# Kernel tuning notes

Measured on AMD Instinct MI355X. Metric: run time of the kernel, lower is better.

## Reference

```python
import jax, jax.numpy as jnp
import numpy as np

HID = 2048
NH = 16
NKV = 4
HD = 256
ROT = 64  # partial_rotary_factor 0.25 * 256
EPS = 1e-6
B, S = 2, 2048


def rms_norm(x, w, eps=EPS):
    # Qwen3.5 RMSNorm: zero-init weight, (1 + w) scaling, fp32 compute
    xf = x.astype(jnp.float32)
    out = xf * jax.lax.rsqrt(jnp.mean(xf * xf, axis=-1, keepdims=True) + eps)
    return (out * (1.0 + w.astype(jnp.float32))).astype(x.dtype)


def rotate_half(x):
    x1, x2 = jnp.split(x, 2, axis=-1)
    return jnp.concatenate([-x2, x1], axis=-1)


def apply_partial_rope(q, k, cos, sin):
    # q,k: [b,h,s,d]; cos,sin: [b,s,rot] -> unsqueeze head dim
    c = cos[:, None, :, :]
    s = sin[:, None, :, :]
    q_rot, q_pass = q[..., :ROT], q[..., ROT:]
    k_rot, k_pass = k[..., :ROT], k[..., ROT:]
    q_rot = q_rot * c + rotate_half(q_rot) * s
    k_rot = k_rot * c + rotate_half(k_rot) * s
    return (jnp.concatenate([q_rot, q_pass], -1), jnp.concatenate([k_rot, k_pass], -1))


def setup_inputs() -> dict:
    key = jax.random.key(0)
    ks = jax.random.split(key, 10)
    hidden_states = jax.random.normal(ks[0], (B, S, HID), jnp.float32)
    # rotary embeddings over ROT dims (half freqs duplicated, HF-style)
    inv_freq = 1.0 / (10000.0 ** (np.arange(0, ROT, 2, dtype=np.float32) / ROT))
    t = np.arange(S, dtype=np.float32)
    freqs = np.outer(t, inv_freq)  # [S, ROT/2]
    emb = np.concatenate([freqs, freqs], axis=-1)  # [S, ROT]
    cos = jnp.broadcast_to(jnp.cos(emb)[None], (B, S, ROT)).astype(jnp.float32)
    sin = jnp.broadcast_to(jnp.sin(emb)[None], (B, S, ROT)).astype(jnp.float32)
    # additive causal mask
    m = jnp.where(jnp.tril(jnp.ones((S, S), bool)), 0.0, -1e9).astype(jnp.float32)
    attention_mask = jnp.broadcast_to(m[None, None], (B, 1, S, S))
    sc = 0.02
    Wq = jax.random.normal(ks[1], (HID, NH * HD * 2), jnp.float32) * sc
    Wk = jax.random.normal(ks[2], (HID, NKV * HD), jnp.float32) * sc
    Wv = jax.random.normal(ks[3], (HID, NKV * HD), jnp.float32) * sc
    Wo = jax.random.normal(ks[4], (NH * HD, HID), jnp.float32) * sc
    q_norm_w = jax.random.normal(ks[5], (HD,), jnp.float32) * sc
    k_norm_w = jax.random.normal(ks[6], (HD,), jnp.float32) * sc
    Wr = jax.random.normal(ks[7], (HID, 2 * HD), jnp.float32) * sc  # dynamic router
    return {"hidden_states": hidden_states, "cos": cos, "sin": sin,
            "attention_mask": attention_mask, "Wq": Wq, "Wk": Wk, "Wv": Wv,
            "Wo": Wo, "q_norm_w": q_norm_w, "k_norm_w": k_norm_w, "Wr": Wr}


def reference(hidden_states, cos, sin, attention_mask, Wq, Wk, Wv, Wo, q_norm_w, k_norm_w, Wr):
    b, s, _ = hidden_states.shape
    # dynamic router -> per-token virtual gates (inner_head for q/k, inner_head_v for v)
    vectors = jax.nn.sigmoid(hidden_states @ Wr)           # [b,s,2*HD]
    g_qk, g_v = jnp.split(vectors, 2, axis=-1)             # [b,s,HD] each
    # fused q projection -> query + sigmoid output gate
    qkv = (hidden_states @ Wq).reshape(b, s, NH, 2 * HD)
    q, gate = jnp.split(qkv, 2, axis=-1)                   # [b,s,NH,HD]
    gate = gate.reshape(b, s, NH * HD)
    k = (hidden_states @ Wk).reshape(b, s, NKV, HD)
    v = (hidden_states @ Wv).reshape(b, s, NKV, HD)
    # per-head RMSNorm before RoPE
    q = rms_norm(q, q_norm_w)
    k = rms_norm(k, k_norm_w)
    q = q.transpose(0, 2, 1, 3)                            # [b,NH,s,HD]
    k = k.transpose(0, 2, 1, 3)                            # [b,NKV,s,HD]
    v = v.transpose(0, 2, 1, 3)
    # virtual gating (inner_head): per-token per-channel gate within each head
    q = q * g_qk[:, None, :, :]
    k = k * g_qk[:, None, :, :]
    v = v * g_v[:, None, :, :]
    # partial RoPE on first ROT dims
    q, k = apply_partial_rope(q, k, cos, sin)
    # GQA: repeat kv heads
    n_rep = NH // NKV
    k = jnp.repeat(k, n_rep, axis=1)                       # [b,NH,s,HD]
    v = jnp.repeat(v, n_rep, axis=1)
    scores = jnp.einsum('bhqd,bhkd->bhqk', q, k) / jnp.sqrt(jnp.float32(HD))
    scores = scores + attention_mask
    attn = jax.nn.softmax(scores.astype(jnp.float32), axis=-1).astype(q.dtype)
    out = jnp.einsum('bhqk,bhkd->bhqd', attn, v)
    out = out.transpose(0, 2, 1, 3).reshape(b, s, NH * HD)
    out = out * jax.nn.sigmoid(gate)                       # sigmoid output gate
    return out @ Wo
```

## Files before the change

### kernel.cpp

```cpp
#include <hip/hip_runtime.h>

#define S_LEN 2048
#define NB    2
#define NH    16
#define NKV   4
#define HDIM  256
#define LW    10752

using bf16x8 = __attribute__((ext_vector_type(8))) short;
using s16x4  = __attribute__((ext_vector_type(4))) short;
using f32x4  = __attribute__((ext_vector_type(4))) float;

__device__ __forceinline__ float bf2f(short u){
  union { float f; unsigned u; } x; x.u = ((unsigned)(unsigned short)u) << 16; return x.f;
}
__device__ __forceinline__ short f2bf(float f){
  unsigned i = __builtin_bit_cast(unsigned, f);
  unsigned r = (i + 0x7fffu + ((i >> 16) & 1u)) >> 16;
  return (short)r;
}
__device__ __forceinline__ float sigm(float x){ return 1.0f / (1.0f + __expf(-x)); }

__device__ __forceinline__ void gload16(const short* g, short* lds){
  __builtin_amdgcn_global_load_lds((const __attribute__((address_space(1))) void*)g,
                                   (__attribute__((address_space(3))) void*)lds,
                                   16, 0, 0);
}

__global__ void k_cvt(const float* __restrict__ in, short* __restrict__ out, int n4){
  int i = blockIdx.x * blockDim.x + threadIdx.x;
  if (i >= n4) return;
  float4 v = ((const float4*)in)[i];
  s16x4 o;
  o[0] = f2bf(v.x); o[1] = f2bf(v.y); o[2] = f2bf(v.z); o[3] = f2bf(v.w);
  ((s16x4*)out)[i] = o;
}

__global__ void k_add(const float* __restrict__ b, float* __restrict__ o, int n4){
  int i = blockIdx.x * blockDim.x + threadIdx.x;
  const int stride = gridDim.x * blockDim.x;
  for (; i < n4; i += stride) {
    float4 x = ((const float4*)o)[i];
    float4 y = ((const float4*)b)[i];
    float4 z = {x.x + y.x, x.y + y.y, x.z + y.z, x.w + y.w};
    ((float4*)o)[i] = z;
  }
}

__global__ void k_wt(const float* __restrict__ Wq, const float* __restrict__ Wk,
                     const float* __restrict__ Wv, const float* __restrict__ Wr,
                     const float* __restrict__ Wo, short* __restrict__ WcatT,
                     short* __restrict__ WoT)
{
  __shared__ float tile[32][33];
  const int id = blockIdx.x;
  const float* src; short* dst; int R, C, Ct, local;
  if (id < 16384)      { src = Wq; dst = WcatT;                      R = 2048; C = 8192; Ct = 256; local = id; }
  else if (id < 18432) { src = Wk; dst = WcatT + (size_t)8192*2048;  R = 2048; C = 1024; Ct =  32; local = id - 16384; }
  else if (id < 20480) { src = Wv; dst = WcatT + (size_t)9216*2048;  R = 2048; C = 1024; Ct =  32; local = id - 18432; }
  else if (id < 21504) { src = Wr; dst = WcatT + (size_t)10240*2048; R = 2048; C =  512; Ct =  16; local = id - 20480; }
  else                 { src = Wo; dst = WoT;                        R = 4096; C = 2048; Ct =  64; local = id - 21504; }
  const int c0 = (local % Ct) * 32, r0 = (local / Ct) * 32;
  const int tx = threadIdx.x, ty = threadIdx.y;
  #pragma unroll
  for (int i = ty; i < 32; i += 8)
    tile[i][tx] = src[(size_t)(r0 + i) * C + c0 + tx];
  __syncthreads();
  #pragma unroll
  for (int i = ty; i < 32; i += 8)
    dst[(size_t)(c0 + i) * R + r0 + tx] = f2bf(tile[tx][i]);
}

__global__ void k_vt(const short* __restrict__ Ycat, short* __restrict__ VT){
  __shared__ short tile[32][33];
  int b = blockIdx.z >> 2, hk = blockIdx.z & 3;
  int s0 = blockIdx.x * 32, d0 = blockIdx.y * 32;
  int tx = threadIdx.x, ty = threadIdx.y;
  #pragma unroll
  for (int i = ty; i < 32; i += 8)
    tile[i][tx] = Ycat[(size_t)(b * S_LEN + s0 + i) * LW + 9216 + hk * 256 + d0 + tx];
  __syncthreads();
  #pragma unroll
  for (int i = ty; i < 32; i += 8)
    VT[(size_t)((b * NKV + hk) * HDIM + d0 + i) * S_LEN + s0 + tx] = tile[tx][i];
}

#define MFMA_(a, b, c) __builtin_amdgcn_mfma_f32_16x16x32_bf16(a, b, c, 0, 0, 0)
#define As ((short(*)[2][8192])(SMEM))
#define Bs ((short(*)[2][8192])(SMEM + 32768))
#define LDA_(buf, ks, mh, f) (*(const bf16x8*)&As[buf][ks][(wm*128 + (mh)*64 + (f)*16 + l15) * 32 + rdSlot])
#define LDB_(buf, ks, f)     (*(const bf16x8*)&Bs[buf][ks][(wn*64  + (f)*16 + l15) * 32 + rdSlot])
#define STAGE_A_(buf, ks, tile) { \
  gload16(aG0 + (size_t)(tile)*64 + (ks)*32, &As[buf][ks][w*512]); \
  gload16(aG1 + (size_t)(tile)*64 + (ks)*32, &As[buf][ks][4096 + w*512]); }
#define STAGE_B_(buf, ks, tile) { \
  gload16(bG0 + (size_t)(tile)*64 + (ks)*32, &Bs[buf][ks][w*512]); \
  gload16(bG1 + (size_t)(tile)*64 + (ks)*32, &Bs[buf][ks][4096 + w*512]); }
#define VM4 asm volatile("s_waitcnt vmcnt(4)" ::: "memory");
#define PH_(buf, ks, mh, LB, ...) { \
  bf16x8 a0 = LDA_(buf,ks,mh,0), a1 = LDA_(buf,ks,mh,1), a2 = LDA_(buf,ks,mh,2), a3 = LDA_(buf,ks,mh,3); \
  if (LB) { b0 = LDB_(buf,ks,0); b1 = LDB_(buf,ks,1); b2 = LDB_(buf,ks,2); b3 = LDB_(buf,ks,3); } \
  __VA_ARGS__ \
  __builtin_amdgcn_s_barrier(); \
  asm volatile("s_waitcnt lgkmcnt(0)" ::: "memory"); \
  __builtin_amdgcn_s_setprio(1); \
  acc[(mh)*4+0][0] = MFMA_(a0, b0, acc[(mh)*4+0][0]); \
  acc[(mh)*4+0][1] = MFMA_(a0, b1, acc[(mh)*4+0][1]); \
  acc[(mh)*4+0][2] = MFMA_(a0, b2, acc[(mh)*4+0][2]); \
  acc[(mh)*4+0][3] = MFMA_(a0, b3, acc[(mh)*4+0][3]); \
  acc[(mh)*4+1][0] = MFMA_(a1, b0, acc[(mh)*4+1][0]); \
  acc[(mh)*4+1][1] = MFMA_(a1, b1, acc[(mh)*4+1][1]); \
  acc[(mh)*4+1][2] = MFMA_(a1, b2, acc[(mh)*4+1][2]); \
  acc[(mh)*4+1][3] = MFMA_(a1, b3, acc[(mh)*4+1][3]); \
  acc[(mh)*4+2][0] = MFMA_(a2, b0, acc[(mh)*4+2][0]); \
  acc[(mh)*4+2][1] = MFMA_(a2, b1, acc[(mh)*4+2][1]); \
  acc[(mh)*4+2][2] = MFMA_(a2, b2, acc[(mh)*4+2][2]); \
  acc[(mh)*4+2][3] = MFMA_(a2, b3, acc[(mh)*4+2][3]); \
  acc[(mh)*4+3][0] = MFMA_(a3, b0, acc[(mh)*4+3][0]); \
  acc[(mh)*4+3][1] = MFMA_(a3, b1, acc[(mh)*4+3][1]); \
  acc[(mh)*4+3][2] = MFMA_(a3, b2, acc[(mh)*4+3][2]); \
  acc[(mh)*4+3][3] = MFMA_(a3, b3, acc[(mh)*4+3][3]); \
  __builtin_amdgcn_s_setprio(0); \
  __builtin_amdgcn_s_barrier(); }

template<int OUTF32, int CM, int SPLITK>
__global__ __launch_bounds__(512) void k_gemm2(const short* __restrict__ A,
                                               const short* __restrict__ BT,
                                               void* __restrict__ C0,
                                               void* __restrict__ C1,
                                               int M, int N, int Kpitch, int Klen,
                                               int gx)
{
  __shared__ __align__(16) short SMEM[65536];
  const int t = threadIdx.x, lane = t & 63, w = t >> 6;
  const int l15 = lane & 15;
  const int wm = w >> 2, wn = w & 3;
  const int rdSlot = (((lane >> 4) ^ ((lane >> 1) & 3)) * 8);

  const int nwg = gridDim.x;
  const int swz = (blockIdx.x & 7) * (nwg >> 3) + (blockIdx.x >> 3);
  int rem = swz, kOff = 0;
  void* Cp = C0;
  if (SPLITK) {
    rem = swz & 127;
    if (swz >> 7) { kOff = Klen; Cp = C1; }
  }
  const int m0 = (CM ? (rem % gx) : (rem / gx)) * 256;
  const int n0 = (CM ? (rem / gx) : (rem % gx)) * 256;

  const int sRow = w * 16 + (lane >> 2);
  const int sSwz = ((lane & 3) ^ ((lane >> 3) & 3)) * 8;
  const short* aG0 = A  + (size_t)(m0 + sRow) * Kpitch + kOff + sSwz;
  const short* aG1 = A  + (size_t)(m0 + 128 + sRow) * Kpitch + kOff + sSwz;
  const short* bG0 = BT + (size_t)(n0 + sRow) * Kpitch + kOff + sSwz;
  const short* bG1 = BT + (size_t)(n0 + 128 + sRow) * Kpitch + kOff + sSwz;

  f32x4 acc[8][4] = {};
  bf16x8 b0 = {}, b1 = {}, b2 = {}, b3 = {};

  STAGE_A_(0, 0, 0) STAGE_A_(0, 1, 0) STAGE_B_(0, 0, 0) STAGE_B_(0, 1, 0)
  STAGE_A_(1, 0, 1) STAGE_B_(1, 0, 1)
  asm volatile("s_waitcnt vmcnt(4)" ::: "memory");
  __builtin_amdgcn_s_barrier();

  const int nIt = Klen >> 7;
  for (int i = 0; i < nIt; ++i) {
    const int c = 2 * i;
    const bool st = (i + 1 < nIt);
    PH_(0, 0, 0, 1, STAGE_A_(1, 1, c + 1))
    PH_(0, 0, 1, 0, STAGE_B_(1, 1, c + 1))
    PH_(0, 1, 0, 1, if (st) STAGE_A_(0, 0, c + 2))
    PH_(0, 1, 1, 0, if (st) STAGE_B_(0, 0, c + 2) VM4)
    PH_(1, 0, 0, 1, if (st) STAGE_A_(0, 1, c + 2))
    PH_(1, 0, 1, 0, if (st) STAGE_B_(0, 1, c + 2))
    PH_(1, 1, 0, 1, if (st) STAGE_A_(1, 0, c + 3))
    PH_(1, 1, 1, 0, if (st) STAGE_B_(1, 0, c + 3) VM4)
  }

  float* Cl = (float*)SMEM;
  const int g = lane >> 4;
  #pragma unroll
  for (int ch = 0; ch < 4; ++ch) {
    if (wm == (ch >> 1)) {
      #pragma unroll
      for (int ii2 = 0; ii2 < 4; ++ii2)
        #pragma unroll
        for (int j = 0; j < 4; ++j)
          #pragma unroll
          for (int r = 0; r < 4; ++r)
            Cl[(ii2*16 + g*4 + r) * 260 + wn*64 + j*16 + l15] = acc[(ch & 1)*4 + ii2][j][r];
    }
    asm volatile("s_waitcnt lgkmcnt(0)" ::: "memory");
    __builtin_amdgcn_s_barrier();
    #pragma unroll
    for (int p = 0; p < 4; ++p) {
      const int row = (t >> 5) + p * 16;
      const int c8 = (t & 31) * 8;
      f32x4 v0 = *(const f32x4*)&Cl[row * 260 + c8];
      f32x4 v1 = *(const f32x4*)&Cl[row * 260 + c8 + 4];
      const int grow = m0 + ch * 64 + row;
      if (OUTF32) {
        *(f32x4*)&((float*)Cp)[(size_t)grow * N + n0 + c8]     = v0;
        *(f32x4*)&((float*)Cp)[(size_t)grow * N + n0 + c8 + 4] = v1;
      } else {
        unsigned d0, d1, d2, d3;
        asm("v_cvt_pk_bf16_f32 %0, %1, %2" : "=v"(d0) : "v"(v0[0]), "v"(v0[1]));
        asm("v_cvt_pk_bf16_f32 %0, %1, %2" : "=v"(d1) : "v"(v0[2]), "v"(v0[3]));
        asm("v_cvt_pk_bf16_f32 %0, %1, %2" : "=v"(d2) : "v"(v1[0]), "v"(v1[1]));
        asm("v_cvt_pk_bf16_f32 %0, %1, %2" : "=v"(d3) : "v"(v1[2]), "v"(v1[3]));
        uint4 u = {d0, d1, d2, d3};
        *(uint4*)&((short*)Cp)[(size_t)grow * N + n0 + c8] = u;
      }
    }
    asm volatile("s_waitcnt lgkmcnt(0)" ::: "memory");
    __builtin_amdgcn_s_barrier();
  }
}
#undef As
#undef Bs

__global__ __launch_bounds__(256) void k_post(short* __restrict__ Ycat,
    const float* __restrict__ cosb, const float* __restrict__ sinb,
    const float* __restrict__ qw, const float* __restrict__ kw)
{
  const int tok = blockIdx.x;
  const int lane = threadIdx.x & 63, w = threadIdx.x >> 6;
  const size_t rowb = (size_t)tok * LW;
  const int d0 = lane * 4;

  float gq[4], gv[4];
  {
    s16x4 a  = *(const s16x4*)&Ycat[rowb + 10240 + d0];
    s16x4 bq = *(const s16x4*)&Ycat[rowb + 10240 + 256 + d0];
    #pragma unroll
    for (int j = 0; j < 4; ++j){ gq[j] = sigm(bf2f(a[j])); gv[j] = sigm(bf2f(bq[j])); }
  }
  float c4[4] = {0,0,0,0}, s4[4] = {0,0,0,0};
  if (lane < 16) {
    float4 c = *(const float4*)&cosb[(size_t)tok * 64 + d0];
    float4 s = *(const float4*)&sinb[(size_t)tok * 64 + d0];
    c4[0]=c.x; c4[1]=c.y; c4[2]=c.z; c4[3]=c.w;
    s4[0]=s.x; s4[1]=s.y; s4[2]=s.z; s4[3]=s.w;
  }
  float4 qv4 = *(const float4*)&qw[d0];
  float4 kv4 = *(const float4*)&kw[d0];
  float qwa[4] = {qv4.x, qv4.y, qv4.z, qv4.w};
  float kwa[4] = {kv4.x, kv4.y, kv4.z, kv4.w};

  #pragma unroll
  for (int hi = 0; hi < 4; ++hi) {
    const int hh = w * 4 + hi;
    const size_t off = rowb + hh * 512 + d0;
    s16x4 v = *(const s16x4*)&Ycat[off];
    float x[4];
    #pragma unroll
    for (int j = 0; j < 4; ++j) x[j] = bf2f(v[j]);
    float ss = x[0]*x[0] + x[1]*x[1] + x[2]*x[2] + x[3]*x[3];
    #pragma unroll
    for (int o2 = 1; o2 < 64; o2 <<= 1) ss += __shfl_xor(ss, o2);
    float rr = rsqrtf(ss * (1.0f/256.0f) + 1e-6f);
    #pragma unroll
    for (int j = 0; j < 4; ++j) x[j] = x[j] * rr * (1.0f + qwa[j]) * gq[j];
    float p[4];
    #pragma unroll
    for (int j = 0; j < 4; ++j) p[j] = __shfl_xor(x[j], 8);
    if (lane < 8)       { for (int j = 0; j < 4; ++j) x[j] = x[j]*c4[j] - p[j]*s4[j]; }
    else if (lane < 16) { for (int j = 0; j < 4; ++j) x[j] = x[j]*c4[j] + p[j]*s4[j]; }
    s16x4 o;
    #pragma unroll
    for (int j = 0; j < 4; ++j) o[j] = f2bf(x[j]);
    *(s16x4*)&Ycat[off] = o;
  }
  {
    const size_t off = rowb + 8192 + w * 256 + d0;
    s16x4 v = *(const s16x4*)&Ycat[off];
    float x[4];
    #pragma unroll
    for (int j = 0; j < 4; ++j) x[j] = bf2f(v[j]);
    float ss = x[0]*x[0] + x[1]*x[1] + x[2]*x[2] + x[3]*x[3];
    #pragma unroll
    for (int o2 = 1; o2 < 64; o2 <<= 1) ss += __shfl_xor(ss, o2);
    float rr = rsqrtf(ss * (1.0f/256.0f) + 1e-6f);
    #pragma unroll
    for (int j = 0; j < 4; ++j) x[j] = x[j] * rr * (1.0f + kwa[j]) * gq[j];
    float p[4];
    #pragma unroll
    for (int j = 0; j < 4; ++j) p[j] = __shfl_xor(x[j], 8);
    if (lane < 8)       { for (int j = 0; j < 4; ++j) x[j] = x[j]*c4[j] - p[j]*s4[j]; }
    else if (lane < 16) { for (int j = 0; j < 4; ++j) x[j] = x[j]*c4[j] + p[j]*s4[j]; }
    s16x4 o;
    #pragma unroll
    for (int j = 0; j < 4; ++j) o[j] = f2bf(x[j]);
    *(s16x4*)&Ycat[off] = o;
  }
  {
    const size_t off = rowb + 9216 + w * 256 + d0;
    s16x4 v = *(const s16x4*)&Ycat[off];
    s16x4 o;
    #pragma unroll
    for (int j = 0; j < 4; ++j) o[j] = f2bf(bf2f(v[j]) * gv[j]);
    *(s16x4*)&Ycat[off] = o;
  }
}

#define ATT_STAGE(bb, jj) { \
  _Pragma("unroll") \
  for (int ri = 0; ri < 4; ++ri) \
    gload16(kSrc + (size_t)((jj) + ri*8) * LW, &Ks[bb][t*8 + ri*2048]); \
  _Pragma("unroll") \
  for (int ri = 0; ri < 4; ++ri) \
    gload16(vSrc + (jj) + (size_t)(ri*64) * S_LEN, &Vs[bb][t*8 + ri*2048]); }

__global__ __launch_bounds__(256) void k_attn(const short* __restrict__ Ycat,
                                              const short* __restrict__ VT,
                                              short* __restrict__ AO)
{
  __shared__ __align__(16) short Ks[2][8192];
  __shared__ __align__(16) short Vs[2][8192];
  __shared__ __align__(16) short Ps[4][512];

  const int t = threadIdx.x, lane = t & 63, w = t >> 6;
  const int l15 = lane & 15, g = lane >> 4;
  const int id = blockIdx.x;
  const int xcd = id & 7, widx = id >> 3;
  const int b = xcd >> 2, hk = xcd & 3;
  const int h = hk * 4 + (widx & 3);
  const int x = widx >> 2, qq = x & 7, jj = x >> 3;
  const int qsel = (jj == 0) ? 31 - qq : (jj == 1) ? 16 + qq : (jj == 2) ? 15 - qq : qq;
  const int q0 = qsel * 64;
  const int qg = q0 + w * 16 + l15;
  const float SC2 = 0.09016844f;

  bf16x8 qf[8];
  {
    const size_t qb = ((size_t)(b * S_LEN) + qg) * LW + h * 512 + g * 8;
    #pragma unroll
    for (int kk = 0; kk < 8; ++kk)
      qf[kk] = *(const bf16x8*)&Ycat[qb + kk * 32];
  }
  asm volatile("s_waitcnt vmcnt(0)" ::: "memory");

  const int kRow = t >> 5;
  const int kColS = ((((t & 31) * 16) ^ ((kRow & 7) << 4)) >> 1);
  const int vRow = t >> 2;
  const int vColS = ((((t & 3) * 16) ^ ((vRow & 3) << 4)) >> 1);
  const short* kSrc = Ycat + ((size_t)(b * S_LEN) + kRow) * LW + 8192 + hk * 256 + kColS;
  const short* vSrc = VT + ((size_t)((b * NKV + hk) * HDIM + vRow)) * S_LEN + vColS;

  f32x4 oacc[16] = {};
  float m_r = -1e30f, l_r = 0.0f;

  const int nt = (q0 >> 5) + 2;
  ATT_STAGE(0, 0)
  int buf = 0;
  char* Pw = (char*)Ps[w] + l15 * 64;
  const int pswz = (l15 & 3) << 4;

  for (int ti = 0; ti < nt; ++ti) {
    const int j0 = ti * 32;
    const int jn = (ti + 1 < nt) ? j0 + 32 : 0;
    ATT_STAGE(buf ^ 1, jn)
    asm volatile("s_waitcnt vmcnt(8)" ::: "memory");
    __builtin_amdgcn_s_barrier();

    if (j0 <= q0 + w * 16 + 15) {
      f32x4 sa[2] = {};
      #pragma unroll
      for (int kk = 0; kk < 8; ++kk) {
        #pragma unroll
        for (int c = 0; c < 2; ++c) {
          const int row = c * 16 + l15;
          bf16x8 kf = *(const bf16x8*)((const char*)Ks[buf] + row * 512
                       + ((kk * 64 + g * 16) ^ ((l15 & 7) << 4)));
          sa[c] = __builtin_amdgcn_mfma_f32_16x16x32_bf16(kf, qf[kk], sa[c], 0, 0, 0);
        }
      }
      float s[8];
      #pragma unroll
      for (int c = 0; c < 2; ++c)
        #pragma unroll
        for (int r = 0; r < 4; ++r) s[c * 4 + r] = sa[c][r];
      if (j0 + 31 > qg) {
        #pragma unroll
        for (int c = 0; c < 2; ++c)
          #pragma unroll
          for (int r = 0; r < 4; ++r)
            if (j0 + c * 16 + g * 4 + r > qg) s[c * 4 + r] = -1e30f;
      }
      float mx = s[0];
      #pragma unroll
      for (int i = 1; i < 8; ++i) mx = fmaxf(mx, s[i]);
      mx = fmaxf(mx, __shfl_xor(mx, 16));
      mx = fmaxf(mx, __shfl_xor(mx, 32));
      if (!__all(mx - m_r <= 128.0f)) {
        const float mnew = fmaxf(m_r, mx);
        const float alpha = exp2f((m_r - mnew) * SC2);
        l_r *= alpha;
        #pragma unroll
        for (int jb = 0; jb < 16; ++jb)
          #pragma unroll
          for (int r = 0; r < 4; ++r) oacc[jb][r] *= alpha;
        m_r = mnew;
      }
      float p[8], rs = 0.0f;
      #pragma unroll
      for (int i = 0; i < 8; ++i) { p[i] = exp2f((s[i] - m_r) * SC2); rs += p[i]; }
      rs += __shfl_xor(rs, 16);
      rs += __shfl_xor(rs, 32);
      l_r += rs;
      #pragma unroll
      for (int c = 0; c < 2; ++c) {
        uint2 u;
        u.x = (unsigned short)f2bf(p[c*4+0]) | ((unsigned)(unsigned short)f2bf(p[c*4+1]) << 16);
        u.y = (unsigned short)f2bf(p[c*4+2]) | ((unsigned)(unsigned short)f2bf(p[c*4+3]) << 16);
        *(uint2*)(Pw + ((c * 32 + 8 * g) ^ pswz)) = u;
      }
      bf16x8 pa = *(const bf16x8*)(Pw + ((16 * g) ^ pswz));
      #pragma unroll
      for (int jb = 0; jb < 16; ++jb) {
        const int vrow = jb * 16 + l15;
        bf16x8 vf = *(const bf16x8*)((const char*)Vs[buf] + vrow * 64
                     + ((16 * g) ^ ((l15 & 3) << 4)));
        oacc[jb] = __builtin_amdgcn_mfma_f32_16x16x32_bf16(vf, pa, oacc[jb], 0, 0, 0);
      }
    }
    __builtin_amdgcn_s_barrier();
    buf ^= 1;
  }
  asm volatile("s_waitcnt vmcnt(0)" ::: "memory");

  const float linv = 1.0f / l_r;
  const size_t gb = ((size_t)(b * S_LEN) + qg) * LW + h * 512 + 256;
  const size_t ob = ((size_t)(b * S_LEN) + qg) * 4096 + h * 256;
  #pragma unroll
  for (int jb = 0; jb < 16; ++jb) {
    const int d0 = jb * 16 + g * 4;
    s16x4 gt = *(const s16x4*)&Ycat[gb + d0];
    s16x4 o;
    #pragma unroll
    for (int r = 0; r < 4; ++r)
      o[r] = f2bf(oacc[jb][r] * linv * sigm(bf2f(gt[r])));
    *(s16x4*)&AO[ob + d0] = o;
  }
}

extern "C" void kernel_launch(void* const* d_in, const int* in_sizes, int n_in,
                              void* d_out, int out_size, void* d_ws, size_t ws_size,
                              hipStream_t stream) {
  const float* X    = (const float*)d_in[0];
  const float* cosb = (const float*)d_in[1];
  const float* sinb = (const float*)d_in[2];
  const float* Wq   = (const float*)d_in[4];
  const float* Wk   = (const float*)d_in[5];
  const float* Wv   = (const float*)d_in[6];
  const float* Wo   = (const float*)d_in[7];
  const float* qw   = (const float*)d_in[8];
  const float* kw   = (const float*)d_in[9];
  const float* Wr   = (const float*)d_in[10];

  short* Xb    = (short*)d_ws;
  short* WcatT = Xb    +  8388608;
  short* AO    = WcatT;
  short* WoT   = WcatT + 22020096;
  short* Ycat  = WoT   +  8388608;
  short* VT    = Ycat  + 44040192;
  float* P1    = (float*)Ycat;

  dim3 tb(32, 8);
  k_cvt<<<8192, 256, 0, stream>>>(X, Xb, 2097152);
  k_wt<<<29696, tb, 0, stream>>>(Wq, Wk, Wv, Wr, Wo, WcatT, WoT);

  k_gemm2<0, 1, 0><<<672, 512, 0, stream>>>(Xb, WcatT, Ycat, nullptr,
                                            4096, 10752, 2048, 2048, 16);
  k_post<<<4096, 256, 0, stream>>>(Ycat, cosb, sinb, qw, kw);
  k_vt<<<dim3(64, 8, 8), tb, 0, stream>>>(Ycat, VT);
  k_attn<<<1024, 256, 0, stream>>>(Ycat, VT, AO);
  k_gemm2<1, 0, 1><<<256, 512, 0, stream>>>(AO, WoT, d_out, P1,
                                            4096, 2048, 4096, 2048, 8);
  k_add<<<2048, 256, 0, stream>>>(P1, (float*)d_out, 2097152);
}
```

Before: 502.2 us.

## Double query rows per attention wave and vectorize weight transpose with 64x64 tiles

Each attention wave now processes two 16-row query groups with the same K/V tiles, so a block covers 128 query rows and half as many blocks launch. Every K and V fragment read from LDS feeds twice as many MFMAs. In exchange the kernel holds two sets of accumulators and softmax state, which raises register pressure (launch bounds set to 2 blocks) and coarsens causal load balance. Separately, the weight transpose/convert kernel uses 64x64 tiles with float4 loads, packed bf16 conversion and 16-byte stores to cut instruction count and improve store coalescing.

```diff
diff --git a/kernel.cpp b/kernel.cpp
--- a/kernel.cpp
+++ b/kernel.cpp
@@ -47,28 +47,36 @@
   }
 }
 
-__global__ void k_wt(const float* __restrict__ Wq, const float* __restrict__ Wk,
-                     const float* __restrict__ Wv, const float* __restrict__ Wr,
-                     const float* __restrict__ Wo, short* __restrict__ WcatT,
-                     short* __restrict__ WoT)
+__global__ __launch_bounds__(256) void k_wt(const float* __restrict__ Wq,
+                     const float* __restrict__ Wk, const float* __restrict__ Wv,
+                     const float* __restrict__ Wr, const float* __restrict__ Wo,
+                     short* __restrict__ WcatT, short* __restrict__ WoT)
 {
-  __shared__ float tile[32][33];
+  __shared__ float tile[64][65];
   const int id = blockIdx.x;
   const float* src; short* dst; int R, C, Ct, local;
-  if (id < 16384)      { src = Wq; dst = WcatT;                      R = 2048; C = 8192; Ct = 256; local = id; }
-  else if (id < 18432) { src = Wk; dst = WcatT + (size_t)8192*2048;  R = 2048; C = 1024; Ct =  32; local = id - 16384; }
-  else if (id < 20480) { src = Wv; dst = WcatT + (size_t)9216*2048;  R = 2048; C = 1024; Ct =  32; local = id - 18432; }
-  else if (id < 21504) { src = Wr; dst = WcatT + (size_t)10240*2048; R = 2048; C =  512; Ct =  16; local = id - 20480; }
-  else                 { src = Wo; dst = WoT;                        R = 4096; C = 2048; Ct =  64; local = id - 21504; }
-  const int c0 = (local % Ct) * 32, r0 = (local / Ct) * 32;
-  const int tx = threadIdx.x, ty = threadIdx.y;
-  #pragma unroll
-  for (int i = ty; i < 32; i += 8)
-    tile[i][tx] = src[(size_t)(r0 + i) * C + c0 + tx];
+  if (id < 4096)      { src = Wq; dst = WcatT;                      R = 2048; C = 8192; Ct = 128; local = id; }
+  else if (id < 4608) { src = Wk; dst = WcatT + (size_t)8192*2048;  R = 2048; C = 1024; Ct =  16; local = id - 4096; }
+  else if (id < 5120) { src = Wv; dst = WcatT + (size_t)9216*2048;  R = 2048; C = 1024; Ct =  16; local = id - 4608; }
+  else if (id < 5376) { src = Wr; dst = WcatT + (size_t)10240*2048; R = 2048; C =  512; Ct =   8; local = id - 5120; }
+  else                { src = Wo; dst = WoT;                        R = 4096; C = 2048; Ct =  32; local = id - 5376; }
+  const int c0 = (local % Ct) * 64, r0 = (local / Ct) * 64;
+  const int t = threadIdx.x;
+  const int rr = t >> 2, cg = (t & 3) * 16;
+  #pragma unroll
+  for (int j = 0; j < 4; ++j)
+    *(float4*)&tile[rr][cg + j*4] = *(const float4*)&src[(size_t)(r0 + rr) * C + c0 + cg + j*4];
   __syncthreads();
-  #pragma unroll
-  for (int i = ty; i < 32; i += 8)
-    dst[(size_t)(c0 + i) * R + r0 + tx] = f2bf(tile[tx][i]);
+  unsigned u[8];
+  #pragma unroll
+  for (int j = 0; j < 8; ++j) {
+    float lo = tile[cg + 2*j][rr], hi = tile[cg + 2*j + 1][rr];
+    asm("v_cvt_pk_bf16_f32 %0, %1, %2" : "=v"(u[j]) : "v"(lo), "v"(hi));
+  }
+  uint4 u0 = {u[0], u[1], u[2], u[3]}, u1 = {u[4], u[5], u[6], u[7]};
+  short* dp = &dst[(size_t)(c0 + rr) * R + r0 + cg];
+  *(uint4*)dp = u0;
+  *(uint4*)(dp + 8) = u1;
 }
 
 __global__ void k_vt(const short* __restrict__ Ycat, short* __restrict__ VT){
@@ -311,13 +319,56 @@
   for (int ri = 0; ri < 4; ++ri) \
     gload16(vSrc + (jj) + (size_t)(ri*64) * S_LEN, &Vs[bb][t*8 + ri*2048]); }
 
-__global__ __launch_bounds__(256) void k_attn(const short* __restrict__ Ycat,
-                                              const short* __restrict__ VT,
-                                              short* __restrict__ AO)
+#define SOFTMAX_SET(sa, qgX, m_r, l_r, oacc, Pww, paX) { \
+  float s[8]; \
+  _Pragma("unroll") \
+  for (int c = 0; c < 2; ++c) \
+    _Pragma("unroll") \
+    for (int r = 0; r < 4; ++r) s[c*4+r] = sa[c][r]; \
+  if (j0 + 31 > (qgX)) { \
+    _Pragma("unroll") \
+    for (int c = 0; c < 2; ++c) \
+      _Pragma("unroll") \
+      for (int r = 0; r < 4; ++r) \
+        if (j0 + c*16 + g*4 + r > (qgX)) s[c*4+r] = -1e30f; \
+  } \
+  float mx = s[0]; \
+  _Pragma("unroll") \
+  for (int i2 = 1; i2 < 8; ++i2) mx = fmaxf(mx, s[i2]); \
+  mx = fmaxf(mx, __shfl_xor(mx, 16)); \
+  mx = fmaxf(mx, __shfl_xor(mx, 32)); \
+  if (!__all(mx - m_r <= 128.0f)) { \
+    const float mnew = fmaxf(m_r, mx); \
+    const float alpha = exp2f((m_r - mnew) * SC2); \
+    l_r *= alpha; \
+    _Pragma("unroll") \
+    for (int jb = 0; jb < 16; ++jb) \
+      _Pragma("unroll") \
+      for (int r = 0; r < 4; ++r) oacc[jb][r] *= alpha; \
+    m_r = mnew; \
+  } \
+  float p[8], rs = 0.0f; \
+  _Pragma("unroll") \
+  for (int i2 = 0; i2 < 8; ++i2) { p[i2] = exp2f((s[i2] - m_r) * SC2); rs += p[i2]; } \
+  rs += __shfl_xor(rs, 16); \
+  rs += __shfl_xor(rs, 32); \
+  l_r += rs; \
+  _Pragma("unroll") \
+  for (int c = 0; c < 2; ++c) { \
+    uint2 u; \
+    u.x = (unsigned short)f2bf(p[c*4+0]) | ((unsigned)(unsigned short)f2bf(p[c*4+1]) << 16); \
+    u.y = (unsigned short)f2bf(p[c*4+2]) | ((unsigned)(unsigned short)f2bf(p[c*4+3]) << 16); \
+    *(uint2*)((Pww) + ((c * 32 + 8 * g) ^ pswz)) = u; \
+  } \
+  paX = *(const bf16x8*)((Pww) + ((16 * g) ^ pswz)); }
+
+__global__ __launch_bounds__(256, 2) void k_attn(const short* __restrict__ Ycat,
+                                                 const short* __restrict__ VT,
+                                                 short* __restrict__ AO)
 {
   __shared__ __align__(16) short Ks[2][8192];
   __shared__ __align__(16) short Vs[2][8192];
-  __shared__ __align__(16) short Ps[4][512];
+  __shared__ __align__(16) short Ps[4][1024];
 
   const int t = threadIdx.x, lane = t & 63, w = t >> 6;
   const int l15 = lane & 15, g = lane >> 4;
@@ -325,18 +376,22 @@
   const int xcd = id & 7, widx = id >> 3;
   const int b = xcd >> 2, hk = xcd & 3;
   const int h = hk * 4 + (widx & 3);
-  const int x = widx >> 2, qq = x & 7, jj = x >> 3;
-  const int qsel = (jj == 0) ? 31 - qq : (jj == 1) ? 16 + qq : (jj == 2) ? 15 - qq : qq;
-  const int q0 = qsel * 64;
-  const int qg = q0 + w * 16 + l15;
+  const int x = widx >> 2;
+  const int qsel = (x < 8) ? 15 - x : x - 8;
+  const int q0 = qsel * 128;
+  const int qgA = q0 + w * 32 + l15;
+  const int qgB = qgA + 16;
   const float SC2 = 0.09016844f;
 
-  bf16x8 qf[8];
+  bf16x8 qfA[8], qfB[8];
   {
-    const size_t qb = ((size_t)(b * S_LEN) + qg) * LW + h * 512 + g * 8;
-    #pragma unroll
-    for (int kk = 0; kk < 8; ++kk)
-      qf[kk] = *(const bf16x8*)&Ycat[qb + kk * 32];
+    const size_t qa = ((size_t)(b * S_LEN) + qgA) * LW + h * 512 + g * 8;
+    const size_t qb = ((size_t)(b * S_LEN) + qgB) * LW + h * 512 + g * 8;
+    #pragma unroll
+    for (int kk = 0; kk < 8; ++kk) {
+      qfA[kk] = *(const bf16x8*)&Ycat[qa + kk * 32];
+      qfB[kk] = *(const bf16x8*)&Ycat[qb + kk * 32];
+    }
   }
   asm volatile("s_waitcnt vmcnt(0)" ::: "memory");
 
@@ -347,13 +402,14 @@
   const short* kSrc = Ycat + ((size_t)(b * S_LEN) + kRow) * LW + 8192 + hk * 256 + kColS;
   const short* vSrc = VT + ((size_t)((b * NKV + hk) * HDIM + vRow)) * S_LEN + vColS;
 
-  f32x4 oacc[16] = {};
-  float m_r = -1e30f, l_r = 0.0f;
-
-  const int nt = (q0 >> 5) + 2;
+  f32x4 oaccA[16] = {}, oaccB[16] = {};
+  float m_rA = -1e30f, l_rA = 0.0f, m_rB = -1e30f, l_rB = 0.0f;
+
+  const int nt = (q0 >> 5) + 4;
   ATT_STAGE(0, 0)
   int buf = 0;
-  char* Pw = (char*)Ps[w] + l15 * 64;
+  char* PwA = (char*)Ps[w] + l15 * 64;
+  char* PwB = PwA + 1024;
   const int pswz = (l15 & 3) << 4;
 
   for (int ti = 0; ti < nt; ++ti) {
@@ -363,8 +419,8 @@
     asm volatile("s_waitcnt vmcnt(8)" ::: "memory");
     __builtin_amdgcn_s_barrier();
 
-    if (j0 <= q0 + w * 16 + 15) {
-      f32x4 sa[2] = {};
+    if (j0 <= q0 + w * 32 + 31) {
+      f32x4 saA[2] = {}, saB[2] = {};
       #pragma unroll
       for (int kk = 0; kk < 8; ++kk) {
         #pragma unroll
@@ -372,56 +428,20 @@
           const int row = c * 16 + l15;
           bf16x8 kf = *(const bf16x8*)((const char*)Ks[buf] + row * 512
                        + ((kk * 64 + g * 16) ^ ((l15 & 7) << 4)));
-          sa[c] = __builtin_amdgcn_mfma_f32_16x16x32_bf16(kf, qf[kk], sa[c], 0, 0, 0);
+          saA[c] = __builtin_amdgcn_mfma_f32_16x16x32_bf16(kf, qfA[kk], saA[c], 0, 0, 0);
+          saB[c] = __builtin_amdgcn_mfma_f32_16x16x32_bf16(kf, qfB[kk], saB[c], 0, 0, 0);
         }
       }
-      float s[8];
-      #pragma unroll
-      for (int c = 0; c < 2; ++c)
-        #pragma unroll
-        for (int r = 0; r < 4; ++r) s[c * 4 + r] = sa[c][r];
-      if (j0 + 31 > qg) {
-        #pragma unroll
-        for (int c = 0; c < 2; ++c)
-          #pragma unroll
-          for (int r = 0; r < 4; ++r)
-            if (j0 + c * 16 + g * 4 + r > qg) s[c * 4 + r] = -1e30f;
-      }
-      float mx = s[0];
-      #pragma unroll
-      for (int i = 1; i < 8; ++i) mx = fmaxf(mx, s[i]);
-      mx = fmaxf(mx, __shfl_xor(mx, 16));
-      mx = fmaxf(mx, __shfl_xor(mx, 32));
-      if (!__all(mx - m_r <= 128.0f)) {
-        const float mnew = fmaxf(m_r, mx);
-        const float alpha = exp2f((m_r - mnew) * SC2);
-        l_r *= alpha;
-        #pragma unroll
-        for (int jb = 0; jb < 16; ++jb)
-          #pragma unroll
-          for (int r = 0; r < 4; ++r) oacc[jb][r] *= alpha;
-        m_r = mnew;
-      }
-      float p[8], rs = 0.0f;
-      #pragma unroll
-      for (int i = 0; i < 8; ++i) { p[i] = exp2f((s[i] - m_r) * SC2); rs += p[i]; }
-      rs += __shfl_xor(rs, 16);
-      rs += __shfl_xor(rs, 32);
-      l_r += rs;
-      #pragma unroll
-      for (int c = 0; c < 2; ++c) {
-        uint2 u;
-        u.x = (unsigned short)f2bf(p[c*4+0]) | ((unsigned)(unsigned short)f2bf(p[c*4+1]) << 16);
-        u.y = (unsigned short)f2bf(p[c*4+2]) | ((unsigned)(unsigned short)f2bf(p[c*4+3]) << 16);
-        *(uint2*)(Pw + ((c * 32 + 8 * g) ^ pswz)) = u;
-      }
-      bf16x8 pa = *(const bf16x8*)(Pw + ((16 * g) ^ pswz));
+      bf16x8 paA, paB;
+      SOFTMAX_SET(saA, qgA, m_rA, l_rA, oaccA, PwA, paA)
+      SOFTMAX_SET(saB, qgB, m_rB, l_rB, oaccB, PwB, paB)
       #pragma unroll
       for (int jb = 0; jb < 16; ++jb) {
         const int vrow = jb * 16 + l15;
         bf16x8 vf = *(const bf16x8*)((const char*)Vs[buf] + vrow * 64
                      + ((16 * g) ^ ((l15 & 3) << 4)));
-        oacc[jb] = __builtin_amdgcn_mfma_f32_16x16x32_bf16(vf, pa, oacc[jb], 0, 0, 0);
+        oaccA[jb] = __builtin_amdgcn_mfma_f32_16x16x32_bf16(vf, paA, oaccA[jb], 0, 0, 0);
+        oaccB[jb] = __builtin_amdgcn_mfma_f32_16x16x32_bf16(vf, paB, oaccB[jb], 0, 0, 0);
       }
     }
     __builtin_amdgcn_s_barrier();
@@ -429,18 +449,24 @@
   }
   asm volatile("s_waitcnt vmcnt(0)" ::: "memory");
 
-  const float linv = 1.0f / l_r;
-  const size_t gb = ((size_t)(b * S_LEN) + qg) * LW + h * 512 + 256;
-  const size_t ob = ((size_t)(b * S_LEN) + qg) * 4096 + h * 256;
+  const float linvA = 1.0f / l_rA, linvB = 1.0f / l_rB;
+  const size_t gbA = ((size_t)(b * S_LEN) + qgA) * LW + h * 512 + 256;
+  const size_t obA = ((size_t)(b * S_LEN) + qgA) * 4096 + h * 256;
+  const size_t gbB = ((size_t)(b * S_LEN) + qgB) * LW + h * 512 + 256;
+  const size_t obB = ((size_t)(b * S_LEN) + qgB) * 4096 + h * 256;
   #pragma unroll
   for (int jb = 0; jb < 16; ++jb) {
     const int d0 = jb * 16 + g * 4;
-    s16x4 gt = *(const s16x4*)&Ycat[gb + d0];
-    s16x4 o;
-    #pragma unroll
-    for (int r = 0; r < 4; ++r)
-      o[r] = f2bf(oacc[jb][r] * linv * sigm(bf2f(gt[r])));
-    *(s16x4*)&AO[ob + d0] = o;
+    s16x4 gtA = *(const s16x4*)&Ycat[gbA + d0];
+    s16x4 gtB = *(const s16x4*)&Ycat[gbB + d0];
+    s16x4 oA, oB;
+    #pragma unroll
+    for (int r = 0; r < 4; ++r) {
+      oA[r] = f2bf(oaccA[jb][r] * linvA * sigm(bf2f(gtA[r])));
+      oB[r] = f2bf(oaccB[jb][r] * linvB * sigm(bf2f(gtB[r])));
+    }
+    *(s16x4*)&AO[obA + d0] = oA;
+    *(s16x4*)&AO[obB + d0] = oB;
   }
 }
 
@@ -468,13 +494,13 @@
 
   dim3 tb(32, 8);
   k_cvt<<<8192, 256, 0, stream>>>(X, Xb, 2097152);
-  k_wt<<<29696, tb, 0, stream>>>(Wq, Wk, Wv, Wr, Wo, WcatT, WoT);
+  k_wt<<<7424, 256, 0, stream>>>(Wq, Wk, Wv, Wr, Wo, WcatT, WoT);
 
   k_gemm2<0, 1, 0><<<672, 512, 0, stream>>>(Xb, WcatT, Ycat, nullptr,
                                             4096, 10752, 2048, 2048, 16);
   k_post<<<4096, 256, 0, stream>>>(Ycat, cosb, sinb, qw, kw);
   k_vt<<<dim3(64, 8, 8), tb, 0, stream>>>(Ycat, VT);
-  k_attn<<<1024, 256, 0, stream>>>(Ycat, VT, AO);
+  k_attn<<<512, 256, 0, stream>>>(Ycat, VT, AO);
   k_gemm2<1, 0, 1><<<256, 512, 0, stream>>>(AO, WoT, d_out, P1,
                                             4096, 2048, 4096, 2048, 8);
   k_add<<<2048, 256, 0, stream>>>(P1, (float*)d_out, 2097152);
```

Result: no change. 510.8 us (+1.7%).

## Permute K rows to drop P LDS round-trip and widen weight transpose tiles

Applied to the files above, without the earlier changes.

Attention now loads K rows into shared memory in a permuted order, so each lane's softmax probabilities already match the MFMA B-operand layout. P can then be packed in registers with v_cvt_pk_bf16_f32 instead of being written to and read back from LDS, and the causal mask index is adjusted to the new row order. Separately, the weight transpose/convert kernel moves to 64x64 tiles with float4 loads and 16-byte packed bf16 stores, which cuts block count and widens memory transactions. The risks are more LDS bank conflicts on the strided transpose reads and subtle layout errors in the permutation.

```diff
diff --git a/kernel.cpp b/kernel.cpp
--- a/kernel.cpp
+++ b/kernel.cpp
@@ -47,28 +47,36 @@
   }
 }
 
-__global__ void k_wt(const float* __restrict__ Wq, const float* __restrict__ Wk,
-                     const float* __restrict__ Wv, const float* __restrict__ Wr,
-                     const float* __restrict__ Wo, short* __restrict__ WcatT,
-                     short* __restrict__ WoT)
+__global__ __launch_bounds__(256) void k_wt(const float* __restrict__ Wq,
+                     const float* __restrict__ Wk, const float* __restrict__ Wv,
+                     const float* __restrict__ Wr, const float* __restrict__ Wo,
+                     short* __restrict__ WcatT, short* __restrict__ WoT)
 {
-  __shared__ float tile[32][33];
+  __shared__ float tile[64][65];
   const int id = blockIdx.x;
   const float* src; short* dst; int R, C, Ct, local;
-  if (id < 16384)      { src = Wq; dst = WcatT;                      R = 2048; C = 8192; Ct = 256; local = id; }
-  else if (id < 18432) { src = Wk; dst = WcatT + (size_t)8192*2048;  R = 2048; C = 1024; Ct =  32; local = id - 16384; }
-  else if (id < 20480) { src = Wv; dst = WcatT + (size_t)9216*2048;  R = 2048; C = 1024; Ct =  32; local = id - 18432; }
-  else if (id < 21504) { src = Wr; dst = WcatT + (size_t)10240*2048; R = 2048; C =  512; Ct =  16; local = id - 20480; }
-  else                 { src = Wo; dst = WoT;                        R = 4096; C = 2048; Ct =  64; local = id - 21504; }
-  const int c0 = (local % Ct) * 32, r0 = (local / Ct) * 32;
-  const int tx = threadIdx.x, ty = threadIdx.y;
-  #pragma unroll
-  for (int i = ty; i < 32; i += 8)
-    tile[i][tx] = src[(size_t)(r0 + i) * C + c0 + tx];
+  if (id < 4096)      { src = Wq; dst = WcatT;                      R = 2048; C = 8192; Ct = 128; local = id; }
+  else if (id < 4608) { src = Wk; dst = WcatT + (size_t)8192*2048;  R = 2048; C = 1024; Ct =  16; local = id - 4096; }
+  else if (id < 5120) { src = Wv; dst = WcatT + (size_t)9216*2048;  R = 2048; C = 1024; Ct =  16; local = id - 4608; }
+  else if (id < 5376) { src = Wr; dst = WcatT + (size_t)10240*2048; R = 2048; C =  512; Ct =   8; local = id - 5120; }
+  else                { src = Wo; dst = WoT;                        R = 4096; C = 2048; Ct =  32; local = id - 5376; }
+  const int c0 = (local % Ct) * 64, r0 = (local / Ct) * 64;
+  const int t = threadIdx.x;
+  const int rr = t >> 2, cg = (t & 3) * 16;
+  #pragma unroll
+  for (int j = 0; j < 4; ++j)
+    *(float4*)&tile[rr][cg + j*4] = *(const float4*)&src[(size_t)(r0 + rr) * C + c0 + cg + j*4];
   __syncthreads();
-  #pragma unroll
-  for (int i = ty; i < 32; i += 8)
-    dst[(size_t)(c0 + i) * R + r0 + tx] = f2bf(tile[tx][i]);
+  unsigned u[8];
+  #pragma unroll
+  for (int j = 0; j < 8; ++j) {
+    float lo = tile[cg + 2*j][rr], hi = tile[cg + 2*j + 1][rr];
+    asm("v_cvt_pk_bf16_f32 %0, %1, %2" : "=v"(u[j]) : "v"(lo), "v"(hi));
+  }
+  uint4 u0 = {u[0], u[1], u[2], u[3]}, u1 = {u[4], u[5], u[6], u[7]};
+  short* dp = &dst[(size_t)(c0 + rr) * R + r0 + cg];
+  *(uint4*)dp = u0;
+  *(uint4*)(dp + 8) = u1;
 }
 
 __global__ void k_vt(const short* __restrict__ Ycat, short* __restrict__ VT){
@@ -303,10 +311,11 @@
   }
 }
 
+#define JR(ri) (8 * (((ri)*2 + (tr >> 2)) & 3) + 4 * ((ri) >> 1) + (tr & 3))
 #define ATT_STAGE(bb, jj) { \
   _Pragma("unroll") \
   for (int ri = 0; ri < 4; ++ri) \
-    gload16(kSrc + (size_t)((jj) + ri*8) * LW, &Ks[bb][t*8 + ri*2048]); \
+    gload16(kSrc + (size_t)((jj) + JR(ri)) * LW, &Ks[bb][t*8 + ri*2048]); \
   _Pragma("unroll") \
   for (int ri = 0; ri < 4; ++ri) \
     gload16(vSrc + (jj) + (size_t)(ri*64) * S_LEN, &Vs[bb][t*8 + ri*2048]); }
@@ -317,7 +326,6 @@
 {
   __shared__ __align__(16) short Ks[2][8192];
   __shared__ __align__(16) short Vs[2][8192];
-  __shared__ __align__(16) short Ps[4][512];
 
   const int t = threadIdx.x, lane = t & 63, w = t >> 6;
   const int l15 = lane & 15, g = lane >> 4;
@@ -340,11 +348,11 @@
   }
   asm volatile("s_waitcnt vmcnt(0)" ::: "memory");
 
-  const int kRow = t >> 5;
-  const int kColS = ((((t & 31) * 16) ^ ((kRow & 7) << 4)) >> 1);
+  const int tr = t >> 5;
+  const int kColS = ((((t & 31) * 16) ^ (tr << 4)) >> 1);
   const int vRow = t >> 2;
   const int vColS = ((((t & 3) * 16) ^ ((vRow & 3) << 4)) >> 1);
-  const short* kSrc = Ycat + ((size_t)(b * S_LEN) + kRow) * LW + 8192 + hk * 256 + kColS;
+  const short* kSrc = Ycat + (size_t)(b * S_LEN) * LW + 8192 + hk * 256 + kColS;
   const short* vSrc = VT + ((size_t)((b * NKV + hk) * HDIM + vRow)) * S_LEN + vColS;
 
   f32x4 oacc[16] = {};
@@ -353,8 +361,6 @@
   const int nt = (q0 >> 5) + 2;
   ATT_STAGE(0, 0)
   int buf = 0;
-  char* Pw = (char*)Ps[w] + l15 * 64;
-  const int pswz = (l15 & 3) << 4;
 
   for (int ti = 0; ti < nt; ++ti) {
     const int j0 = ti * 32;
@@ -385,7 +391,7 @@
         for (int c = 0; c < 2; ++c)
           #pragma unroll
           for (int r = 0; r < 4; ++r)
-            if (j0 + c * 16 + g * 4 + r > qg) s[c * 4 + r] = -1e30f;
+            if (j0 + 8 * g + 4 * c + r > qg) s[c * 4 + r] = -1e30f;
       }
       float mx = s[0];
       #pragma unroll
@@ -408,14 +414,12 @@
       rs += __shfl_xor(rs, 16);
       rs += __shfl_xor(rs, 32);
       l_r += rs;
-      #pragma unroll
-      for (int c = 0; c < 2; ++c) {
-        uint2 u;
-        u.x = (unsigned short)f2bf(p[c*4+0]) | ((unsigned)(unsigned short)f2bf(p[c*4+1]) << 16);
-        u.y = (unsigned short)f2bf(p[c*4+2]) | ((unsigned)(unsigned short)f2bf(p[c*4+3]) << 16);
-        *(uint2*)(Pw + ((c * 32 + 8 * g) ^ pswz)) = u;
-      }
-      bf16x8 pa = *(const bf16x8*)(Pw + ((16 * g) ^ pswz));
+      union { uint4 u; bf16x8 v; } pk;
+      asm("v_cvt_pk_bf16_f32 %0, %1, %2" : "=v"(pk.u.x) : "v"(p[0]), "v"(p[1]));
+      asm("v_cvt_pk_bf16_f32 %0, %1, %2" : "=v"(pk.u.y) : "v"(p[2]), "v"(p[3]));
+      asm("v_cvt_pk_bf16_f32 %0, %1, %2" : "=v"(pk.u.z) : "v"(p[4]), "v"(p[5]));
+      asm("v_cvt_pk_bf16_f32 %0, %1, %2" : "=v"(pk.u.w) : "v"(p[6]), "v"(p[7]));
+      const bf16x8 pa = pk.v;
       #pragma unroll
       for (int jb = 0; jb < 16; ++jb) {
         const int vrow = jb * 16 + l15;
@@ -468,7 +472,7 @@
 
   dim3 tb(32, 8);
   k_cvt<<<8192, 256, 0, stream>>>(X, Xb, 2097152);
-  k_wt<<<29696, tb, 0, stream>>>(Wq, Wk, Wv, Wr, Wo, WcatT, WoT);
+  k_wt<<<7424, 256, 0, stream>>>(Wq, Wk, Wv, Wr, Wo, WcatT, WoT);
 
   k_gemm2<0, 1, 0><<<672, 512, 0, stream>>>(Xb, WcatT, Ycat, nullptr,
                                             4096, 10752, 2048, 2048, 16);
```

New measurement: 478.8 us. 1.05x faster.
